# Kernel optimization log

Hardware: AMD Instinct MI355X
Metric: run time of the kernel (lower is better)

The kernel has to match this reference:

```python
import jax, jax.numpy as jnp
import numpy as np

N_NODES = 100000
N_EDGES = 1600000
IN_CH = 256
OUT_CH = 64
ITERATIONS = 4


def setup_inputs() -> dict:
    key = jax.random.key(0)
    k1, k2, k3, k4, k5 = jax.random.split(key, 5)
    adj_index = jax.random.randint(k1, (2, N_EDGES), 0, N_NODES, dtype=jnp.int64)
    adj_values = jax.random.uniform(k2, (N_EDGES,), dtype=jnp.float32)
    features = jax.random.normal(k3, (N_NODES, IN_CH), dtype=jnp.float32)
    # Xavier-uniform init as in the torch module
    bw = float(np.sqrt(6.0 / (IN_CH + OUT_CH)))
    weight = jax.random.uniform(k4, (IN_CH, OUT_CH), dtype=jnp.float32, minval=-bw, maxval=bw)
    bb = float(np.sqrt(6.0 / (1 + OUT_CH)))
    bias = jax.random.uniform(k5, (1, OUT_CH), dtype=jnp.float32, minval=-bb, maxval=bb)
    return {"adj_index": adj_index, "adj_values": adj_values, "features": features,
            "weight": weight, "bias": bias}


def reference(adj_index, adj_values, features, weight, bias):
    # Dense transform: [N, in] @ [in, out] + [1, out], then ReLU (dropout = identity in eval)
    base = jax.nn.relu(features @ weight + bias)  # [N, out]
    rows = adj_index[0]  # destination rows of A (output index of SpMM)
    cols = adj_index[1]  # source columns of A (gather index)
    n = base.shape[0]
    # (iterations - 1) hops of SpMM: base <- A @ base
    for _ in range(ITERATIONS - 1):
        msgs = adj_values[:, None] * base[cols]           # [E, out] gather + scale
        base = jax.ops.segment_sum(msgs, rows, num_segments=n)  # [N, out] scatter-add
    return base
```

## Files before the change

### kernel.cpp

```cpp
#include <hip/hip_runtime.h>
#include <hip/hip_bf16.h>

#define IN_CH 256
#define OUT_CH 64
#define NFMAX 512
#define RPB 256
#define CHUNK 6144
#define CAP 8192

__device__ __forceinline__ unsigned short f2bf(float f) {
    unsigned u = __float_as_uint(f);
    u += 0x7fff + ((u >> 16) & 1);
    return (unsigned short)(u >> 16);
}
__device__ __forceinline__ unsigned short f2bf_hw(float f) {
    __hip_bfloat16 h = __float2bfloat16(f);
    union { __hip_bfloat16 b; unsigned short u; } c;
    c.b = h;
    return c.u;
}
__device__ __forceinline__ float bf2f(unsigned short h) {
    return __uint_as_float((unsigned)h << 16);
}

struct Edge12 { int r; int c; float v; };

using bfrag = __attribute__((ext_vector_type(8))) short;
using ffrag = __attribute__((ext_vector_type(4))) float;

__global__ __launch_bounds__(256) void wprep_kernel(
    const float* __restrict__ W, unsigned short* __restrict__ Wf)
{
    int i = blockIdx.x * 256 + threadIdx.x;
    int k  = i >> 6;
    int c  = i & 63;
    int ks = k >> 5;
    int kq = (k >> 3) & 3;
    int j  = k & 7;
    int nt = c >> 4;
    int lc = c & 15;
    Wf[(((ks * 4 + nt) * 64) + kq * 16 + lc) * 8 + j] = f2bf(W[i]);
}

__global__ __launch_bounds__(256) void gemm_mfma_kernel(
    const float* __restrict__ feat, const unsigned short* __restrict__ Wf,
    const float* __restrict__ bias, unsigned short* __restrict__ out, int n)
{
    const int wv   = threadIdx.x >> 6;
    const int lane = threadIdx.x & 63;
    const int quad = lane >> 4;
    const int lc   = lane & 15;

    const int rbase = blockIdx.x * 128 + wv * 32;
    const int lrow0 = min(rbase + lc,      n - 1);
    const int lrow1 = min(rbase + 16 + lc, n - 1);
    const float4* frow0 = (const float4*)(feat + (size_t)lrow0 * IN_CH);
    const float4* frow1 = (const float4*)(feat + (size_t)lrow1 * IN_CH);

    ffrag acc0[4], acc1[4];
#pragma unroll
    for (int nt = 0; nt < 4; ++nt)
#pragma unroll
        for (int r = 0; r < 4; ++r) { acc0[nt][r] = 0.f; acc1[nt][r] = 0.f; }

#pragma unroll
    for (int ks = 0; ks < 8; ++ks) {
        float4 a00 = frow0[ks * 8 + quad * 2 + 0];
        float4 a01 = frow0[ks * 8 + quad * 2 + 1];
        float4 a10 = frow1[ks * 8 + quad * 2 + 0];
        float4 a11 = frow1[ks * 8 + quad * 2 + 1];
        bfrag af0, af1;
        af0[0] = (short)f2bf_hw(a00.x); af0[1] = (short)f2bf_hw(a00.y);
        af0[2] = (short)f2bf_hw(a00.z); af0[3] = (short)f2bf_hw(a00.w);
        af0[4] = (short)f2bf_hw(a01.x); af0[5] = (short)f2bf_hw(a01.y);
        af0[6] = (short)f2bf_hw(a01.z); af0[7] = (short)f2bf_hw(a01.w);
        af1[0] = (short)f2bf_hw(a10.x); af1[1] = (short)f2bf_hw(a10.y);
        af1[2] = (short)f2bf_hw(a10.z); af1[3] = (short)f2bf_hw(a10.w);
        af1[4] = (short)f2bf_hw(a11.x); af1[5] = (short)f2bf_hw(a11.y);
        af1[6] = (short)f2bf_hw(a11.z); af1[7] = (short)f2bf_hw(a11.w);
#pragma unroll
        for (int nt = 0; nt < 4; ++nt) {
            bfrag bf = *(const bfrag*)&Wf[(((ks * 4 + nt) * 64) + lane) * 8];
            acc0[nt] = __builtin_amdgcn_mfma_f32_16x16x32_bf16(af0, bf, acc0[nt], 0, 0, 0);
            acc1[nt] = __builtin_amdgcn_mfma_f32_16x16x32_bf16(af1, bf, acc1[nt], 0, 0, 0);
        }
    }

#pragma unroll
    for (int nt = 0; nt < 4; ++nt) {
        float bv = bias[nt * 16 + lc];
#pragma unroll
        for (int r = 0; r < 4; ++r) {
            int orow0 = rbase + quad * 4 + r;
            int orow1 = rbase + 16 + quad * 4 + r;
            if (orow0 < n) {
                float v = fmaxf(acc0[nt][r] + bv, 0.f);
                out[(size_t)orow0 * OUT_CH + nt * 16 + lc] = f2bf_hw(v);
            }
            if (orow1 < n) {
                float v = fmaxf(acc1[nt][r] + bv, 0.f);
                out[(size_t)orow1 * OUT_CH + nt * 16 + lc] = f2bf_hw(v);
            }
        }
    }
}

__global__ __launch_bounds__(256) void fine_count_kernel(
    const int* __restrict__ rows, int* __restrict__ fineCnt,
    int nEdges, int nfine)
{
    __shared__ int h[NFMAX];
    const int t = threadIdx.x;
    for (int i = t; i < nfine; i += 256) h[i] = 0;
    __syncthreads();
    const int stride = gridDim.x * 256;
    for (int e = blockIdx.x * 256 + t; e < nEdges; e += stride)
        atomicAdd(&h[__builtin_nontemporal_load(rows + e) >> 8], 1);
    __syncthreads();
    for (int i = t; i < nfine; i += 256) {
        int v = h[i];
        if (v) atomicAdd(&fineCnt[i], v);
    }
}

__global__ __launch_bounds__(256) void fine_scan_kernel(
    const int* __restrict__ fineCnt, int* __restrict__ fineBase,
    int* __restrict__ flushCursor, int* __restrict__ rowptr,
    int n, int nfine, int E)
{
    __shared__ int tmp[256];
    const int t = threadIdx.x;
    int a = (2 * t     < nfine) ? fineCnt[2 * t]     : 0;
    int b = (2 * t + 1 < nfine) ? fineCnt[2 * t + 1] : 0;
    tmp[t] = a + b;
    __syncthreads();
    for (int off = 1; off < 256; off <<= 1) {
        int x = (t >= off) ? tmp[t - off] : 0;
        __syncthreads();
        tmp[t] += x;
        __syncthreads();
    }
    int excl = tmp[t] - (a + b);
    if (2 * t < nfine)     { fineBase[2 * t]     = excl;     flushCursor[2 * t]     = excl;     }
    if (2 * t + 1 < nfine) { fineBase[2 * t + 1] = excl + a; flushCursor[2 * t + 1] = excl + a; }
    if (t == 0) { fineBase[nfine] = E; rowptr[n] = E; }
}

__global__ __launch_bounds__(256) void fine_scatter_kernel(
    const int* __restrict__ rows, const int* __restrict__ cols,
    const float* __restrict__ vals, int* __restrict__ flushCursor,
    Edge12* __restrict__ eb, int nEdges, int nfine)
{
    __shared__ int hist[NFMAX];
    __shared__ int lofs[NFMAX];
    __shared__ int gpos[NFMAX];
    __shared__ int cur[NFMAX];
    __shared__ int scanTmp[256];
    __shared__ int   sr[CHUNK];
    __shared__ int   sc[CHUNK];
    __shared__ float sv[CHUNK];

    const int t  = threadIdx.x;
    const int e0 = blockIdx.x * CHUNK;
    const int cnt_in = min(CHUNK, nEdges - e0);

    for (int i = t; i < nfine; i += 256) hist[i] = 0;
    __syncthreads();

    int   lr[CHUNK / 256];
    int   lc[CHUNK / 256];
    float lv[CHUNK / 256];
#pragma unroll
    for (int j = 0; j < CHUNK / 256; ++j) {
        int i = j * 256 + t;
        if (i < cnt_in) {
            lr[j] = __builtin_nontemporal_load(rows + e0 + i);
            lc[j] = __builtin_nontemporal_load(cols + e0 + i);
            lv[j] = __builtin_nontemporal_load(vals + e0 + i);
            atomicAdd(&hist[lr[j] >> 8], 1);
        } else {
            lr[j] = -1;
        }
    }
    __syncthreads();

    int a  = (2 * t     < nfine) ? hist[2 * t]     : 0;
    int b2 = (2 * t + 1 < nfine) ? hist[2 * t + 1] : 0;
    scanTmp[t] = a + b2;
    __syncthreads();
    for (int off = 1; off < 256; off <<= 1) {
        int x = (t >= off) ? scanTmp[t - off] : 0;
        __syncthreads();
        scanTmp[t] += x;
        __syncthreads();
    }
    int excl = scanTmp[t] - (a + b2);
    if (2 * t < nfine)     lofs[2 * t]     = excl;
    if (2 * t + 1 < nfine) lofs[2 * t + 1] = excl + a;
    __syncthreads();

    for (int i = t; i < nfine; i += 256) {
        int h = hist[i];
        gpos[i] = h ? atomicAdd(&flushCursor[i], h) : 0;
        cur[i]  = lofs[i];
    }
    __syncthreads();

#pragma unroll
    for (int j = 0; j < CHUNK / 256; ++j) {
        if (lr[j] >= 0) {
            int bk = lr[j] >> 8;
            int p  = atomicAdd(&cur[bk], 1);
            sr[p] = lr[j];
            sc[p] = lc[j];
            sv[p] = lv[j];
        }
    }
    __syncthreads();

    for (int i = t; i < cnt_in; i += 256) {
        int bk = sr[i] >> 8;
        int p  = gpos[bk] + (i - lofs[bk]);
        eb[p].r = sr[i];
        eb[p].c = sc[i];
        eb[p].v = sv[i];
    }
}

__global__ __launch_bounds__(256) void bucket_sort_kernel(
    const Edge12* __restrict__ eb, const int* __restrict__ fineBase,
    int2* __restrict__ spack, int* __restrict__ rowptr, int n)
{
    __shared__ int  rowCnt[RPB];
    __shared__ int  rowStart[RPB + 1];
    __shared__ int  scanTmp[RPB];
    __shared__ int  winEnd;
    __shared__ int2 st[CAP];

    const int bkt = blockIdx.x;
    const int t   = threadIdx.x;
    const int lo  = fineBase[bkt];
    const int hi  = fineBase[bkt + 1];
    const int r0  = bkt << 8;

    rowCnt[t] = 0;
    __syncthreads();
    for (int e = lo + t; e < hi; e += 256)
        atomicAdd(&rowCnt[eb[e].r - r0], 1);
    __syncthreads();

    int v = rowCnt[t];
    scanTmp[t] = v;
    __syncthreads();
    for (int off = 1; off < 256; off <<= 1) {
        int x = (t >= off) ? scanTmp[t - off] : 0;
        __syncthreads();
        scanTmp[t] += x;
        __syncthreads();
    }
    rowStart[t + 1] = scanTmp[t];
    if (t == 0) rowStart[0] = 0;
    __syncthreads();

    if (r0 + t < n) rowptr[r0 + t] = lo + rowStart[t];

    int rs = 0;
    while (rs < RPB) {
        if (t == 0) {
            int base = rowStart[rs];
            if (rowStart[rs + 1] - base > CAP) {
                winEnd = -(rs + 1);
            } else {
                int re = rs;
                while (re < RPB && rowStart[re + 1] - base <= CAP) ++re;
                winEnd = re;
            }
        }
        __syncthreads();
        int  re     = winEnd;
        bool direct = false;
        if (re < 0) { re = -re; direct = true; }
        const int base = rowStart[rs];
        const int cnt  = rowStart[re] - base;

        if (t >= rs && t < re) rowCnt[t] = rowStart[t] - base;
        __syncthreads();

        if (!direct) {
            for (int e = lo + t; e < hi; e += 256) {
                Edge12 ed = eb[e];
                int rl = ed.r - r0;
                if (rl >= rs && rl < re) {
                    int p = atomicAdd(&rowCnt[rl], 1);
                    st[p] = make_int2(ed.c, __float_as_int(ed.v));
                }
            }
            __syncthreads();
            for (int i = t; i < cnt; i += 256)
                spack[lo + base + i] = st[i];
        } else {
            for (int e = lo + t; e < hi; e += 256) {
                Edge12 ed = eb[e];
                if (ed.r - r0 == rs) {
                    int p = atomicAdd(&rowCnt[rs], 1);
                    spack[lo + base + p] = make_int2(ed.c, __float_as_int(ed.v));
                }
            }
        }
        __syncthreads();
        rs = re;
    }
}

template<bool DST_F32>
__global__ __launch_bounds__(256) void spmm_csr_kernel(
    const int* __restrict__ rowptr, const int2* __restrict__ spack,
    const unsigned short* __restrict__ src, void* __restrict__ dstv, int n)
{
    const int row  = blockIdx.x * 4 + (threadIdx.x >> 6);
    const int lane = threadIdx.x & 63;
    if (row >= n) return;

    const int beg = rowptr[row];
    const int end = rowptr[row + 1];
    const int sub = lane >> 4;
    const int ch  = (lane & 15) * 4;

    float4 acc0 = make_float4(0.f, 0.f, 0.f, 0.f);
    float4 acc1 = make_float4(0.f, 0.f, 0.f, 0.f);

    for (int b = beg; b < end; b += 16) {
        int e0 = b + sub;
        int e1 = b + 4 + sub;
        int e2 = b + 8 + sub;
        int e3 = b + 12 + sub;
        int2 p0 = spack[min(e0, end - 1)];
        int2 p1 = spack[min(e1, end - 1)];
        int2 p2 = spack[min(e2, end - 1)];
        int2 p3 = spack[min(e3, end - 1)];
        float v0 = (e0 < end) ? __int_as_float(p0.y) : 0.f;
        float v1 = (e1 < end) ? __int_as_float(p1.y) : 0.f;
        float v2 = (e2 < end) ? __int_as_float(p2.y) : 0.f;
        float v3 = (e3 < end) ? __int_as_float(p3.y) : 0.f;
        ushort4 s0 = *(const ushort4*)(src + ((size_t)p0.x << 6) + ch);
        ushort4 s1 = *(const ushort4*)(src + ((size_t)p1.x << 6) + ch);
        ushort4 s2 = *(const ushort4*)(src + ((size_t)p2.x << 6) + ch);
        ushort4 s3 = *(const ushort4*)(src + ((size_t)p3.x << 6) + ch);
        acc0.x = fmaf(v0, bf2f(s0.x), acc0.x);
        acc0.y = fmaf(v0, bf2f(s0.y), acc0.y);
        acc0.z = fmaf(v0, bf2f(s0.z), acc0.z);
        acc0.w = fmaf(v0, bf2f(s0.w), acc0.w);
        acc1.x = fmaf(v1, bf2f(s1.x), acc1.x);
        acc1.y = fmaf(v1, bf2f(s1.y), acc1.y);
        acc1.z = fmaf(v1, bf2f(s1.z), acc1.z);
        acc1.w = fmaf(v1, bf2f(s1.w), acc1.w);
        acc0.x = fmaf(v2, bf2f(s2.x), acc0.x);
        acc0.y = fmaf(v2, bf2f(s2.y), acc0.y);
        acc0.z = fmaf(v2, bf2f(s2.z), acc0.z);
        acc0.w = fmaf(v2, bf2f(s2.w), acc0.w);
        acc1.x = fmaf(v3, bf2f(s3.x), acc1.x);
        acc1.y = fmaf(v3, bf2f(s3.y), acc1.y);
        acc1.z = fmaf(v3, bf2f(s3.z), acc1.z);
        acc1.w = fmaf(v3, bf2f(s3.w), acc1.w);
    }

    float4 acc = make_float4(acc0.x + acc1.x, acc0.y + acc1.y,
                             acc0.z + acc1.z, acc0.w + acc1.w);

#pragma unroll
    for (int mask = 16; mask <= 32; mask <<= 1) {
        acc.x += __shfl_xor(acc.x, mask);
        acc.y += __shfl_xor(acc.y, mask);
        acc.z += __shfl_xor(acc.z, mask);
        acc.w += __shfl_xor(acc.w, mask);
    }

    if (lane < 16) {
        if constexpr (DST_F32) {
            *(float4*)((float*)dstv + ((size_t)row << 6) + ch) = acc;
        } else {
            ushort4 o;
            o.x = f2bf_hw(acc.x);
            o.y = f2bf_hw(acc.y);
            o.z = f2bf_hw(acc.z);
            o.w = f2bf_hw(acc.w);
            *(ushort4*)((unsigned short*)dstv + ((size_t)row << 6) + ch) = o;
        }
    }
}

extern "C" void kernel_launch(void* const* d_in, const int* in_sizes, int n_in,
                              void* d_out, int out_size, void* d_ws, size_t ws_size,
                              hipStream_t stream)
{
    const int*   adj  = (const int*)d_in[0];
    const float* vals = (const float*)d_in[1];
    const float* feat = (const float*)d_in[2];
    const float* W    = (const float*)d_in[3];
    const float* bias = (const float*)d_in[4];

    const int E = in_sizes[1];
    const int n = in_sizes[2] / IN_CH;
    const int* rows = adj;
    const int* cols = adj + E;

    const int nfine = (n + RPB - 1) >> 8;

    char* ws = (char*)d_ws;
    size_t off = 0;
    auto alloc = [&](size_t bytes) {
        void* p = ws + off;
        off += (bytes + 255) & ~(size_t)255;
        return p;
    };
    unsigned short* B0 = (unsigned short*)alloc((size_t)n * OUT_CH * sizeof(unsigned short));
    unsigned short* B1 = (unsigned short*)alloc((size_t)n * OUT_CH * sizeof(unsigned short));
    int*   rowptr      = (int*)  alloc((size_t)(n + 1) * sizeof(int));
    int2*  spack       = (int2*) alloc((size_t)E * sizeof(int2));
    int*   fineCnt     = (int*)  alloc(NFMAX * sizeof(int));
    int*   fineBase    = (int*)  alloc((NFMAX + 1) * sizeof(int));
    int*   flushCursor = (int*)  alloc(NFMAX * sizeof(int));
    unsigned short* Wf = (unsigned short*)alloc((size_t)IN_CH * OUT_CH * sizeof(unsigned short));

    Edge12* eb = (Edge12*)B0;

    float* out = (float*)d_out;

    wprep_kernel<<<(IN_CH * OUT_CH) / 256, 256, 0, stream>>>(W, Wf);

    hipMemsetAsync(fineCnt, 0, (size_t)nfine * sizeof(int), stream);
    fine_count_kernel<<<256, 256, 0, stream>>>(rows, fineCnt, E, nfine);
    fine_scan_kernel<<<1, 256, 0, stream>>>(fineCnt, fineBase, flushCursor,
                                            rowptr, n, nfine, E);
    fine_scatter_kernel<<<(E + CHUNK - 1) / CHUNK, 256, 0, stream>>>(
        rows, cols, vals, flushCursor, eb, E, nfine);
    bucket_sort_kernel<<<nfine, 256, 0, stream>>>(eb, fineBase, spack, rowptr, n);

    gemm_mfma_kernel<<<(n + 127) / 128, 256, 0, stream>>>(feat, Wf, bias, B0, n);

    const int hblocks = (n + 3) / 4;
    spmm_csr_kernel<false><<<hblocks, 256, 0, stream>>>(rowptr, spack, B0, B1, n);
    spmm_csr_kernel<false><<<hblocks, 256, 0, stream>>>(rowptr, spack, B1, B0, n);
    spmm_csr_kernel<true><<<hblocks, 256, 0, stream>>>(rowptr, spack, B0, out, n);
}
```

Before: 390.7 us.

## Split edge buffer, preload GEMM rows nontemporally, map one row per quarter-wave in SpMM

The intermediate edge buffer is split from a 12-byte struct into an int2 column/value array plus a byte array of row offsets within the bucket. The bucket sort then reads one byte per edge for counting and filtering instead of the full struct. The GEMM now computes 16 rows per wave instead of 32 and issues all feature loads up front as nontemporal loads. SpMM assigns each 16-lane group its own row, which removes the cross-lane shuffle reduction, but threads handling rows with different degrees may diverge.

```diff
diff --git a/kernel.cpp b/kernel.cpp
--- a/kernel.cpp
+++ b/kernel.cpp
@@ -23,10 +23,9 @@
     return __uint_as_float((unsigned)h << 16);
 }
 
-struct Edge12 { int r; int c; float v; };
-
 using bfrag = __attribute__((ext_vector_type(8))) short;
 using ffrag = __attribute__((ext_vector_type(4))) float;
+using f32x4 = __attribute__((ext_vector_type(4))) float;
 
 __global__ __launch_bounds__(256) void wprep_kernel(
     const float* __restrict__ W, unsigned short* __restrict__ Wf)
@@ -51,38 +50,37 @@
     const int quad = lane >> 4;
     const int lc   = lane & 15;
 
-    const int rbase = blockIdx.x * 128 + wv * 32;
-    const int lrow0 = min(rbase + lc,      n - 1);
-    const int lrow1 = min(rbase + 16 + lc, n - 1);
-    const float4* frow0 = (const float4*)(feat + (size_t)lrow0 * IN_CH);
-    const float4* frow1 = (const float4*)(feat + (size_t)lrow1 * IN_CH);
-
-    ffrag acc0[4], acc1[4];
+    const int rbase = blockIdx.x * 64 + wv * 16;
+    const int lrow  = min(rbase + lc, n - 1);
+    const f32x4* frow = (const f32x4*)(feat + (size_t)lrow * IN_CH);
+
+    f32x4 a[16];
+#pragma unroll
+    for (int i = 0; i < 16; ++i) {
+        int ks = i >> 1;
+        int j  = i & 1;
+        a[i] = __builtin_nontemporal_load(frow + ks * 8 + quad * 2 + j);
+    }
+
+    ffrag acc[4];
 #pragma unroll
     for (int nt = 0; nt < 4; ++nt)
 #pragma unroll
-        for (int r = 0; r < 4; ++r) { acc0[nt][r] = 0.f; acc1[nt][r] = 0.f; }
+        for (int r = 0; r < 4; ++r) acc[nt][r] = 0.f;
 
 #pragma unroll
     for (int ks = 0; ks < 8; ++ks) {
-        float4 a00 = frow0[ks * 8 + quad * 2 + 0];
-        float4 a01 = frow0[ks * 8 + quad * 2 + 1];
-        float4 a10 = frow1[ks * 8 + quad * 2 + 0];
-        float4 a11 = frow1[ks * 8 + quad * 2 + 1];
-        bfrag af0, af1;
-        af0[0] = (short)f2bf_hw(a00.x); af0[1] = (short)f2bf_hw(a00.y);
-        af0[2] = (short)f2bf_hw(a00.z); af0[3] = (short)f2bf_hw(a00.w);
-        af0[4] = (short)f2bf_hw(a01.x); af0[5] = (short)f2bf_hw(a01.y);
-        af0[6] = (short)f2bf_hw(a01.z); af0[7] = (short)f2bf_hw(a01.w);
-        af1[0] = (short)f2bf_hw(a10.x); af1[1] = (short)f2bf_hw(a10.y);
-        af1[2] = (short)f2bf_hw(a10.z); af1[3] = (short)f2bf_hw(a10.w);
-        af1[4] = (short)f2bf_hw(a11.x); af1[5] = (short)f2bf_hw(a11.y);
-        af1[6] = (short)f2bf_hw(a11.z); af1[7] = (short)f2bf_hw(a11.w);
+        f32x4 a0 = a[ks * 2 + 0];
+        f32x4 a1 = a[ks * 2 + 1];
+        bfrag af;
+        af[0] = (short)f2bf_hw(a0[0]); af[1] = (short)f2bf_hw(a0[1]);
+        af[2] = (short)f2bf_hw(a0[2]); af[3] = (short)f2bf_hw(a0[3]);
+        af[4] = (short)f2bf_hw(a1[0]); af[5] = (short)f2bf_hw(a1[1]);
+        af[6] = (short)f2bf_hw(a1[2]); af[7] = (short)f2bf_hw(a1[3]);
 #pragma unroll
         for (int nt = 0; nt < 4; ++nt) {
             bfrag bf = *(const bfrag*)&Wf[(((ks * 4 + nt) * 64) + lane) * 8];
-            acc0[nt] = __builtin_amdgcn_mfma_f32_16x16x32_bf16(af0, bf, acc0[nt], 0, 0, 0);
-            acc1[nt] = __builtin_amdgcn_mfma_f32_16x16x32_bf16(af1, bf, acc1[nt], 0, 0, 0);
+            acc[nt] = __builtin_amdgcn_mfma_f32_16x16x32_bf16(af, bf, acc[nt], 0, 0, 0);
         }
     }
 
@@ -91,15 +89,10 @@
         float bv = bias[nt * 16 + lc];
 #pragma unroll
         for (int r = 0; r < 4; ++r) {
-            int orow0 = rbase + quad * 4 + r;
-            int orow1 = rbase + 16 + quad * 4 + r;
-            if (orow0 < n) {
-                float v = fmaxf(acc0[nt][r] + bv, 0.f);
-                out[(size_t)orow0 * OUT_CH + nt * 16 + lc] = f2bf_hw(v);
-            }
-            if (orow1 < n) {
-                float v = fmaxf(acc1[nt][r] + bv, 0.f);
-                out[(size_t)orow1 * OUT_CH + nt * 16 + lc] = f2bf_hw(v);
+            int orow = rbase + quad * 4 + r;
+            if (orow < n) {
+                float v = fmaxf(acc[nt][r] + bv, 0.f);
+                out[(size_t)orow * OUT_CH + nt * 16 + lc] = f2bf_hw(v);
             }
         }
     }
@@ -149,7 +142,8 @@
 __global__ __launch_bounds__(256) void fine_scatter_kernel(
     const int* __restrict__ rows, const int* __restrict__ cols,
     const float* __restrict__ vals, int* __restrict__ flushCursor,
-    Edge12* __restrict__ eb, int nEdges, int nfine)
+    int2* __restrict__ ebcv, unsigned char* __restrict__ ebr,
+    int nEdges, int nfine)
 {
     __shared__ int hist[NFMAX];
     __shared__ int lofs[NFMAX];
@@ -221,14 +215,14 @@
     for (int i = t; i < cnt_in; i += 256) {
         int bk = sr[i] >> 8;
         int p  = gpos[bk] + (i - lofs[bk]);
-        eb[p].r = sr[i];
-        eb[p].c = sc[i];
-        eb[p].v = sv[i];
+        ebcv[p] = make_int2(sc[i], __float_as_int(sv[i]));
+        ebr[p]  = (unsigned char)(sr[i] & 255);
     }
 }
 
 __global__ __launch_bounds__(256) void bucket_sort_kernel(
-    const Edge12* __restrict__ eb, const int* __restrict__ fineBase,
+    const int2* __restrict__ ebcv, const unsigned char* __restrict__ ebr,
+    const int* __restrict__ fineBase,
     int2* __restrict__ spack, int* __restrict__ rowptr, int n)
 {
     __shared__ int  rowCnt[RPB];
@@ -246,7 +240,7 @@
     rowCnt[t] = 0;
     __syncthreads();
     for (int e = lo + t; e < hi; e += 256)
-        atomicAdd(&rowCnt[eb[e].r - r0], 1);
+        atomicAdd(&rowCnt[ebr[e]], 1);
     __syncthreads();
 
     int v = rowCnt[t];
@@ -288,11 +282,10 @@
 
         if (!direct) {
             for (int e = lo + t; e < hi; e += 256) {
-                Edge12 ed = eb[e];
-                int rl = ed.r - r0;
+                int rl = ebr[e];
                 if (rl >= rs && rl < re) {
                     int p = atomicAdd(&rowCnt[rl], 1);
-                    st[p] = make_int2(ed.c, __float_as_int(ed.v));
+                    st[p] = ebcv[e];
                 }
             }
             __syncthreads();
@@ -300,10 +293,10 @@
                 spack[lo + base + i] = st[i];
         } else {
             for (int e = lo + t; e < hi; e += 256) {
-                Edge12 ed = eb[e];
-                if (ed.r - r0 == rs) {
+                int rl = ebr[e];
+                if (rl == rs) {
                     int p = atomicAdd(&rowCnt[rs], 1);
-                    spack[lo + base + p] = make_int2(ed.c, __float_as_int(ed.v));
+                    spack[lo + base + p] = ebcv[e];
                 }
             }
         }
@@ -317,65 +310,41 @@
     const int* __restrict__ rowptr, const int2* __restrict__ spack,
     const unsigned short* __restrict__ src, void* __restrict__ dstv, int n)
 {
-    const int row  = blockIdx.x * 4 + (threadIdx.x >> 6);
+    const int wid  = threadIdx.x >> 6;
     const int lane = threadIdx.x & 63;
-    if (row >= n) return;
-
-    const int beg = rowptr[row];
-    const int end = rowptr[row + 1];
-    const int sub = lane >> 4;
-    const int ch  = (lane & 15) * 4;
-
-    float4 acc0 = make_float4(0.f, 0.f, 0.f, 0.f);
-    float4 acc1 = make_float4(0.f, 0.f, 0.f, 0.f);
-
-    for (int b = beg; b < end; b += 16) {
-        int e0 = b + sub;
-        int e1 = b + 4 + sub;
-        int e2 = b + 8 + sub;
-        int e3 = b + 12 + sub;
-        int2 p0 = spack[min(e0, end - 1)];
-        int2 p1 = spack[min(e1, end - 1)];
-        int2 p2 = spack[min(e2, end - 1)];
-        int2 p3 = spack[min(e3, end - 1)];
-        float v0 = (e0 < end) ? __int_as_float(p0.y) : 0.f;
-        float v1 = (e1 < end) ? __int_as_float(p1.y) : 0.f;
-        float v2 = (e2 < end) ? __int_as_float(p2.y) : 0.f;
-        float v3 = (e3 < end) ? __int_as_float(p3.y) : 0.f;
-        ushort4 s0 = *(const ushort4*)(src + ((size_t)p0.x << 6) + ch);
-        ushort4 s1 = *(const ushort4*)(src + ((size_t)p1.x << 6) + ch);
-        ushort4 s2 = *(const ushort4*)(src + ((size_t)p2.x << 6) + ch);
-        ushort4 s3 = *(const ushort4*)(src + ((size_t)p3.x << 6) + ch);
-        acc0.x = fmaf(v0, bf2f(s0.x), acc0.x);
-        acc0.y = fmaf(v0, bf2f(s0.y), acc0.y);
-        acc0.z = fmaf(v0, bf2f(s0.z), acc0.z);
-        acc0.w = fmaf(v0, bf2f(s0.w), acc0.w);
-        acc1.x = fmaf(v1, bf2f(s1.x), acc1.x);
-        acc1.y = fmaf(v1, bf2f(s1.y), acc1.y);
-        acc1.z = fmaf(v1, bf2f(s1.z), acc1.z);
-        acc1.w = fmaf(v1, bf2f(s1.w), acc1.w);
-        acc0.x = fmaf(v2, bf2f(s2.x), acc0.x);
-        acc0.y = fmaf(v2, bf2f(s2.y), acc0.y);
-        acc0.z = fmaf(v2, bf2f(s2.z), acc0.z);
-        acc0.w = fmaf(v2, bf2f(s2.w), acc0.w);
-        acc1.x = fmaf(v3, bf2f(s3.x), acc1.x);
-        acc1.y = fmaf(v3, bf2f(s3.y), acc1.y);
-        acc1.z = fmaf(v3, bf2f(s3.z), acc1.z);
-        acc1.w = fmaf(v3, bf2f(s3.w), acc1.w);
-    }
-
-    float4 acc = make_float4(acc0.x + acc1.x, acc0.y + acc1.y,
-                             acc0.z + acc1.z, acc0.w + acc1.w);
-
-#pragma unroll
-    for (int mask = 16; mask <= 32; mask <<= 1) {
-        acc.x += __shfl_xor(acc.x, mask);
-        acc.y += __shfl_xor(acc.y, mask);
-        acc.z += __shfl_xor(acc.z, mask);
-        acc.w += __shfl_xor(acc.w, mask);
-    }
-
-    if (lane < 16) {
+    const int sub  = lane >> 4;
+    const int ch   = (lane & 15) * 4;
+    const int row  = blockIdx.x * 16 + wid * 4 + sub;
+    const bool valid = row < n;
+
+    int beg = 0, end = 0;
+    if (valid) { beg = rowptr[row]; end = rowptr[row + 1]; }
+
+    float4 acc = make_float4(0.f, 0.f, 0.f, 0.f);
+
+    for (int b = beg; b < end; b += 4) {
+        int2  p[4];
+        float v[4];
+#pragma unroll
+        for (int j = 0; j < 4; ++j) {
+            int e = b + j;
+            p[j] = spack[min(e, end - 1)];
+            v[j] = (e < end) ? __int_as_float(p[j].y) : 0.f;
+        }
+        ushort4 s[4];
+#pragma unroll
+        for (int j = 0; j < 4; ++j)
+            s[j] = *(const ushort4*)(src + ((size_t)p[j].x << 6) + ch);
+#pragma unroll
+        for (int j = 0; j < 4; ++j) {
+            acc.x = fmaf(v[j], bf2f(s[j].x), acc.x);
+            acc.y = fmaf(v[j], bf2f(s[j].y), acc.y);
+            acc.z = fmaf(v[j], bf2f(s[j].z), acc.z);
+            acc.w = fmaf(v[j], bf2f(s[j].w), acc.w);
+        }
+    }
+
+    if (valid) {
         if constexpr (DST_F32) {
             *(float4*)((float*)dstv + ((size_t)row << 6) + ch) = acc;
         } else {
@@ -422,7 +391,8 @@
     int*   flushCursor = (int*)  alloc(NFMAX * sizeof(int));
     unsigned short* Wf = (unsigned short*)alloc((size_t)IN_CH * OUT_CH * sizeof(unsigned short));
 
-    Edge12* eb = (Edge12*)B0;
+    int2*          ebcv = (int2*)B0;
+    unsigned char* ebr  = (unsigned char*)(ebcv + E);
 
     float* out = (float*)d_out;
 
@@ -433,12 +403,13 @@
     fine_scan_kernel<<<1, 256, 0, stream>>>(fineCnt, fineBase, flushCursor,
                                             rowptr, n, nfine, E);
     fine_scatter_kernel<<<(E + CHUNK - 1) / CHUNK, 256, 0, stream>>>(
-        rows, cols, vals, flushCursor, eb, E, nfine);
-    bucket_sort_kernel<<<nfine, 256, 0, stream>>>(eb, fineBase, spack, rowptr, n);
-
-    gemm_mfma_kernel<<<(n + 127) / 128, 256, 0, stream>>>(feat, Wf, bias, B0, n);
-
-    const int hblocks = (n + 3) / 4;
+        rows, cols, vals, flushCursor, ebcv, ebr, E, nfine);
+    bucket_sort_kernel<<<nfine, 256, 0, stream>>>(ebcv, ebr, fineBase,
+                                                  spack, rowptr, n);
+
+    gemm_mfma_kernel<<<(n + 63) / 64, 256, 0, stream>>>(feat, Wf, bias, B0, n);
+
+    const int hblocks = (n + 15) / 16;
     spmm_csr_kernel<false><<<hblocks, 256, 0, stream>>>(rowptr, spack, B0, B1, n);
     spmm_csr_kernel<false><<<hblocks, 256, 0, stream>>>(rowptr, spack, B1, B0, n);
     spmm_csr_kernel<true><<<hblocks, 256, 0, stream>>>(rowptr, spack, B0, out, n);
```

Result: faster. 372.8 us (-4.6%).
